# Kernel optimization log

Hardware: AMD Instinct MI355X
Metric: run time of the kernel (lower is better)

## Reference

```python
import jax, jax.numpy as jnp
import numpy as np

N_NODES = 100000


def sage_conv(x, src, dst, Wl, Wr, b):
    # mean-aggregate neighbor (source) features onto destinations
    msg = x[src]                                              # [E, F]
    agg = jax.ops.segment_sum(msg, dst, num_segments=N_NODES)  # [N, F]
    deg = jax.ops.segment_sum(jnp.ones(dst.shape, x.dtype), dst, num_segments=N_NODES)
    agg = agg / jnp.maximum(deg, 1.0)[:, None]
    # PyG SAGEConv: lin_l(aggr) + lin_r(x); bias only on lin_l
    return agg @ Wl.T + x @ Wr.T + b


def setup_inputs() -> dict:
    key = jax.random.key(0)
    ks = jax.random.split(key, 12)
    d, h, c = 128, 128, 6
    s = 1.0 / np.sqrt(d)
    return {
        "x": jax.random.normal(ks[0], (N_NODES, d), jnp.float32),
        "edge_index": jax.random.randint(ks[1], (2, 3200000), 0, N_NODES, jnp.int64),
        "Wl1": jax.random.normal(ks[2], (h, d), jnp.float32) * s,
        "Wr1": jax.random.normal(ks[3], (h, d), jnp.float32) * s,
        "b1": jax.random.normal(ks[4], (h,), jnp.float32) * s,
        "Wl2": jax.random.normal(ks[5], (h, h), jnp.float32) * s,
        "Wr2": jax.random.normal(ks[6], (h, h), jnp.float32) * s,
        "b2": jax.random.normal(ks[7], (h,), jnp.float32) * s,
        "Wl3": jax.random.normal(ks[8], (c, h), jnp.float32) * s,
        "Wr3": jax.random.normal(ks[9], (c, h), jnp.float32) * s,
        "b3": jax.random.normal(ks[10], (c,), jnp.float32) * s,
    }


def reference(x, edge_index, Wl1, Wr1, b1, Wl2, Wr2, b2, Wl3, Wr3, b3):
    src, dst = edge_index[0], edge_index[1]
    h = jax.nn.relu(sage_conv(x, src, dst, Wl1, Wr1, b1))  # dropout = identity (eval)
    h = jax.nn.relu(sage_conv(h, src, dst, Wl2, Wr2, b2))
    return sage_conv(h, src, dst, Wl3, Wr3, b3)  # [N, 6]
```

## Files before the change

### kernel.cpp

```cpp
#include <hip/hip_runtime.h>
#include <hip/hip_bf16.h>

#define N_NODES 100000
#define G_PART 16
#define B_PART 96
#define NPG_PAD 6272
#define A_BLOCKS 1024

__global__ __launch_bounds__(256) void partition_edges(
    const int* __restrict__ src, const int* __restrict__ dst, int E,
    int* __restrict__ bkt, unsigned int* __restrict__ gcur, int cap, int npg) {
    __shared__ int cnt16[G_PART];
    __shared__ unsigned int base16[G_PART];
    __shared__ unsigned int cur16[G_PART];
    int tid = threadIdx.x;
    if (tid < G_PART) cnt16[tid] = 0;
    __syncthreads();
    int per = (E + A_BLOCKS - 1) / A_BLOCKS;
    int beg = blockIdx.x * per;
    int end = min(beg + per, E);
    for (int i = beg + tid; i < end; i += 256) {
        int d = dst[i];
        atomicAdd(&cnt16[d / npg], 1);
    }
    __syncthreads();
    if (tid < G_PART) {
        base16[tid] = atomicAdd(&gcur[tid], (unsigned int)cnt16[tid]);
        cur16[tid] = 0;
    }
    __syncthreads();
    for (int i = beg + tid; i < end; i += 256) {
        int d = dst[i];
        int s = src[i];
        int g = d / npg;
        unsigned int p = base16[g] + atomicAdd(&cur16[g], 1u);
        bkt[(size_t)g * cap + p] = ((d - g * npg) << 17) | s;
    }
}

__global__ __launch_bounds__(256) void count_hist(const int* __restrict__ bkt,
                                                  const unsigned int* __restrict__ gcur,
                                                  int cap, unsigned short* __restrict__ partial,
                                                  int npg, int N) {
    __shared__ int hist[NPG_PAD];
    int g = blockIdx.x & (G_PART - 1);
    int b = blockIdx.x / G_PART;
    int tid = threadIdx.x;
    for (int i = tid; i < npg; i += 256) hist[i] = 0;
    __syncthreads();
    int len = (int)gcur[g];
    int per = (len + B_PART - 1) / B_PART;
    int ibeg = b * per;
    int iend = min(ibeg + per, len);
    const int* bp = bkt + (size_t)g * cap;
    for (int i = ibeg + tid; i < iend; i += 256) {
        int v = __builtin_nontemporal_load(bp + i);
        atomicAdd(&hist[v >> 17], 1);
    }
    __syncthreads();
    size_t base = (size_t)(g * B_PART + b) * npg;
    for (int j = tid; j < npg; j += 256) partial[base + j] = (unsigned short)hist[j];
}

__global__ __launch_bounds__(256) void scan_partials(unsigned short* __restrict__ partial,
                                                     int* __restrict__ cnt,
                                                     int npg, int N) {
    int n = blockIdx.x * 256 + threadIdx.x;
    if (n >= N) return;
    int g = n / npg;
    int i = n - g * npg;
    size_t base = (size_t)g * B_PART * npg + i;
    int run = 0;
#pragma unroll 4
    for (int b = 0; b < B_PART; ++b) {
        size_t idx = base + (size_t)b * npg;
        int t = partial[idx];
        partial[idx] = (unsigned short)run;
        run += t;
    }
    cnt[n] = run;
}

__global__ __launch_bounds__(256) void fill_hist(const int* __restrict__ bkt,
                                                 const unsigned int* __restrict__ gcur,
                                                 int cap,
                                                 const unsigned short* __restrict__ partial,
                                                 const int* __restrict__ row_off,
                                                 int* __restrict__ csr_src,
                                                 int npg, int N) {
    __shared__ int cur[NPG_PAD];
    int g = blockIdx.x & (G_PART - 1);
    int b = blockIdx.x / G_PART;
    int lo = g * npg;
    int tid = threadIdx.x;
    size_t pbase = (size_t)(g * B_PART + b) * npg;
    for (int i = tid; i < npg && lo + i < N; i += 256)
        cur[i] = row_off[lo + i] + (int)partial[pbase + i];
    __syncthreads();
    int len = (int)gcur[g];
    int per = (len + B_PART - 1) / B_PART;
    int ibeg = b * per;
    int iend = min(ibeg + per, len);
    const int* bp = bkt + (size_t)g * cap;
    for (int i = ibeg + tid; i < iend; i += 256) {
        int v = __builtin_nontemporal_load(bp + i);
        int p = atomicAdd(&cur[v >> 17], 1);
        csr_src[p] = v & 0x1FFFF;
    }
}

#define SCHUNK 1024

__global__ __launch_bounds__(256) void scan_blocks(const int* __restrict__ cnt,
                                                   int* __restrict__ row_off,
                                                   int* __restrict__ block_sums, int n) {
    __shared__ int ts[256];
    int tid = threadIdx.x;
    int base = blockIdx.x * SCHUNK + tid * 4;
    int v[4];
    int s = 0;
#pragma unroll
    for (int j = 0; j < 4; ++j) {
        int i = base + j;
        v[j] = (i < n) ? cnt[i] : 0;
        s += v[j];
    }
    ts[tid] = s;
    __syncthreads();
    for (int off = 1; off < 256; off <<= 1) {
        int t = 0;
        if (tid >= off) t = ts[tid - off];
        __syncthreads();
        if (tid >= off) ts[tid] += t;
        __syncthreads();
    }
    int run = (tid > 0) ? ts[tid - 1] : 0;
    if (tid == 255) block_sums[blockIdx.x] = ts[255];
#pragma unroll
    for (int j = 0; j < 4; ++j) {
        int i = base + j;
        if (i < n) row_off[i] = run;
        run += v[j];
    }
}

__global__ __launch_bounds__(256) void scan_sums(int* __restrict__ block_sums, int nb,
                                                 int* __restrict__ row_off, int n) {
    __shared__ int ts[256];
    int tid = threadIdx.x;
    int v = (tid < nb) ? block_sums[tid] : 0;
    ts[tid] = v;
    __syncthreads();
    for (int off = 1; off < 256; off <<= 1) {
        int t = 0;
        if (tid >= off) t = ts[tid - off];
        __syncthreads();
        if (tid >= off) ts[tid] += t;
        __syncthreads();
    }
    if (tid < nb) block_sums[tid] = (tid > 0) ? ts[tid - 1] : 0;
    if (tid == 255) row_off[n] = ts[255];
}

__global__ __launch_bounds__(256) void scan_add(int* __restrict__ row_off,
                                                const int* __restrict__ block_sums, int n) {
    int tid = threadIdx.x;
    int off = block_sums[blockIdx.x];
    int base = blockIdx.x * SCHUNK + tid * 4;
#pragma unroll
    for (int j = 0; j < 4; ++j) {
        int i = base + j;
        if (i < n) row_off[i] += off;
    }
}

__global__ __launch_bounds__(256) void pack_bf16(const float* __restrict__ in,
                                                 uint2* __restrict__ out, int n4) {
    int i = blockIdx.x * 256 + threadIdx.x;
    if (i >= n4) return;
    float4 v = *(const float4*)&in[(size_t)i * 4];
    __hip_bfloat162 p0 = __float22bfloat162_rn(make_float2(v.x, v.y));
    __hip_bfloat162 p1 = __float22bfloat162_rn(make_float2(v.z, v.w));
    uint2 o;
    o.x = *(const uint*)&p0;
    o.y = *(const uint*)&p1;
    out[i] = o;
}

static __device__ inline unsigned short f2bf(float v) {
    __hip_bfloat16 b = __float2bfloat16(v);
    return *(const unsigned short*)&b;
}

__global__ __launch_bounds__(256) void pack_weights(
    const float* __restrict__ Wl1, const float* __restrict__ Wr1,
    const float* __restrict__ Wl2, const float* __restrict__ Wr2,
    const float* __restrict__ Wl3, const float* __restrict__ Wr3,
    unsigned short* __restrict__ Wc1, unsigned short* __restrict__ Wc2,
    unsigned short* __restrict__ W3c) {
    int idx = blockIdx.x * 256 + threadIdx.x;
    if (idx < 32768) {
        int n = idx >> 8, k = idx & 255;
        Wc1[idx] = f2bf((k < 128) ? Wl1[n * 128 + k] : Wr1[n * 128 + (k - 128)]);
    } else if (idx < 65536) {
        int t = idx - 32768;
        int n = t >> 8, k = t & 255;
        Wc2[t] = f2bf((k < 128) ? Wl2[n * 128 + k] : Wr2[n * 128 + (k - 128)]);
    } else if (idx < 65536 + 2048) {
        int t = idx - 65536;
        int n = t >> 7, k = t & 127;
        float v = (n < 6) ? Wl3[n * 128 + k] : ((n < 12) ? Wr3[(n - 6) * 128 + k] : 0.f);
        W3c[t] = f2bf(v);
    }
}

static __device__ inline float2 unpack2(uint v) {
    float2 r;
    r.x = __uint_as_float(v << 16);
    r.y = __uint_as_float(v & 0xffff0000u);
    return r;
}

__global__ __launch_bounds__(256) void agg_bf16(const uint* __restrict__ featb,
                                                const int* __restrict__ row_off,
                                                const int* __restrict__ csr,
                                                uint* __restrict__ outb, int M) {
    int node = blockIdx.x * 4 + (threadIdx.x >> 6);
    if (node >= M) return;
    int lane = threadIdx.x & 63;
    int beg = row_off[node], end = row_off[node + 1];
    float sx = 0.f, sy = 0.f;
    int i = beg;
    for (; i + 4 <= end; i += 4) {
        int s0 = csr[i], s1 = csr[i + 1], s2 = csr[i + 2], s3 = csr[i + 3];
        uint v0 = featb[(size_t)s0 * 64 + lane];
        uint v1 = featb[(size_t)s1 * 64 + lane];
        uint v2 = featb[(size_t)s2 * 64 + lane];
        uint v3 = featb[(size_t)s3 * 64 + lane];
        float2 f0 = unpack2(v0), f1 = unpack2(v1), f2 = unpack2(v2), f3 = unpack2(v3);
        sx += f0.x + f1.x + f2.x + f3.x;
        sy += f0.y + f1.y + f2.y + f3.y;
    }
    for (; i < end; ++i) {
        uint v = featb[(size_t)csr[i] * 64 + lane];
        float2 f = unpack2(v);
        sx += f.x;
        sy += f.y;
    }
    float inv = (end > beg) ? 1.0f / (float)(end - beg) : 0.0f;
    __hip_bfloat162 p = __float22bfloat162_rn(make_float2(sx * inv, sy * inv));
    outb[(size_t)node * 64 + lane] = *(const uint*)&p;
}

typedef __attribute__((ext_vector_type(8))) short bfrag8;
typedef __attribute__((ext_vector_type(4))) float f32x4;

__global__ __launch_bounds__(256) void gemm_mfma(
    const unsigned short* __restrict__ Aagg,
    const unsigned short* __restrict__ Aself,
    const unsigned short* __restrict__ Wc,
    const float* __restrict__ bias,
    unsigned short* __restrict__ outb,
    int M, int relu) {
    int wave = threadIdx.x >> 6;
    int lane = threadIdx.x & 63;
    int m0 = blockIdx.x * 64 + wave * 16;
    int mrow = lane & 15;
    int quad = lane >> 4;
    int row = m0 + mrow;
    int rclamp = (row < M) ? row : 0;

    f32x4 acc[8];
#pragma unroll
    for (int t = 0; t < 8; ++t) acc[t] = (f32x4){0.f, 0.f, 0.f, 0.f};

    const unsigned short* arow0 = Aagg + (size_t)rclamp * 128;
    const unsigned short* arow1 = Aself + (size_t)rclamp * 128;
#pragma unroll
    for (int ks = 0; ks < 8; ++ks) {
        int k0 = ks * 32;
        const unsigned short* ap =
            (k0 < 128) ? (arow0 + k0 + quad * 8) : (arow1 + (k0 - 128) + quad * 8);
        bfrag8 af = *(const bfrag8*)ap;
#pragma unroll
        for (int t = 0; t < 8; ++t) {
            const unsigned short* bp = Wc + (size_t)(t * 16 + mrow) * 256 + k0 + quad * 8;
            bfrag8 bf = *(const bfrag8*)bp;
            acc[t] = __builtin_amdgcn_mfma_f32_16x16x32_bf16(af, bf, acc[t], 0, 0, 0);
        }
    }
#pragma unroll
    for (int t = 0; t < 8; ++t) {
        int col = t * 16 + mrow;
        float bcol = bias[col];
#pragma unroll
        for (int r = 0; r < 4; ++r) {
            int orow = m0 + quad * 4 + r;
            if (orow < M) {
                float v = acc[t][r] + bcol;
                if (relu) v = fmaxf(v, 0.f);
                outb[(size_t)orow * 128 + col] = f2bf(v);
            }
        }
    }
}

__global__ __launch_bounds__(256) void lin3_mfma(
    const unsigned short* __restrict__ h2b,
    const unsigned short* __restrict__ W3c,
    const float* __restrict__ b3,
    unsigned short* __restrict__ zg,
    float* __restrict__ zs,
    int M) {
    int wave = threadIdx.x >> 6;
    int lane = threadIdx.x & 63;
    int m0 = blockIdx.x * 64 + wave * 16;
    int mrow = lane & 15;
    int quad = lane >> 4;
    int row = m0 + mrow;
    int rclamp = (row < M) ? row : 0;
    f32x4 acc = (f32x4){0.f, 0.f, 0.f, 0.f};
    const unsigned short* arow = h2b + (size_t)rclamp * 128;
#pragma unroll
    for (int ks = 0; ks < 4; ++ks) {
        bfrag8 af = *(const bfrag8*)(arow + ks * 32 + quad * 8);
        bfrag8 bf = *(const bfrag8*)(W3c + (size_t)mrow * 128 + ks * 32 + quad * 8);
        acc = __builtin_amdgcn_mfma_f32_16x16x32_bf16(af, bf, acc, 0, 0, 0);
    }
    int col = mrow;
#pragma unroll
    for (int r = 0; r < 4; ++r) {
        int orow = m0 + quad * 4 + r;
        if (orow < M) {
            float v = acc[r];
            if (col < 6) {
                zg[(size_t)orow * 8 + col] = f2bf(v);
            } else if (col < 12) {
                zs[(size_t)orow * 6 + (col - 6)] = v + b3[col - 6];
            }
        }
    }
}

__global__ void out_kernel(const unsigned short* __restrict__ zg,
                           const float* __restrict__ zs,
                           const int* __restrict__ row_off,
                           const int* __restrict__ csr,
                           float* __restrict__ out, int M) {
    int idx = blockIdx.x * blockDim.x + threadIdx.x;
    int node = idx >> 3;
    int j = idx & 7;
    if (node >= M || j >= 6) return;
    int beg = row_off[node], end = row_off[node + 1];
    float acc = 0.f;
    int i = beg;
    for (; i + 4 <= end; i += 4) {
        int s0 = csr[i], s1 = csr[i + 1], s2 = csr[i + 2], s3 = csr[i + 3];
        uint z0 = zg[(size_t)s0 * 8 + j];
        uint z1 = zg[(size_t)s1 * 8 + j];
        uint z2 = zg[(size_t)s2 * 8 + j];
        uint z3 = zg[(size_t)s3 * 8 + j];
        acc += __uint_as_float(z0 << 16) + __uint_as_float(z1 << 16) +
               __uint_as_float(z2 << 16) + __uint_as_float(z3 << 16);
    }
    for (; i < end; ++i) {
        uint z = zg[(size_t)csr[i] * 8 + j];
        acc += __uint_as_float(z << 16);
    }
    float inv = (end > beg) ? 1.0f / (float)(end - beg) : 0.0f;
    out[(size_t)node * 6 + j] = acc * inv + zs[(size_t)node * 6 + j];
}

static inline size_t align_up(size_t x, size_t a) { return (x + a - 1) & ~(a - 1); }

extern "C" void kernel_launch(void* const* d_in, const int* in_sizes, int n_in,
                              void* d_out, int out_size, void* d_ws, size_t ws_size,
                              hipStream_t stream) {
    const float* x = (const float*)d_in[0];
    const int* ei = (const int*)d_in[1];
    const float* Wl1 = (const float*)d_in[2];
    const float* Wr1 = (const float*)d_in[3];
    const float* b1 = (const float*)d_in[4];
    const float* Wl2 = (const float*)d_in[5];
    const float* Wr2 = (const float*)d_in[6];
    const float* b2 = (const float*)d_in[7];
    const float* Wl3 = (const float*)d_in[8];
    const float* Wr3 = (const float*)d_in[9];
    const float* b3 = (const float*)d_in[10];

    const int N = in_sizes[0] / 128;
    const int E = in_sizes[1] / 2;
    const int* src = ei;
    const int* dst = ei + E;

    char* ws = (char*)d_ws;
    size_t off = 0;
    int* cnt = (int*)(ws + off);        off = align_up(off + (size_t)N * 4, 512);
    int* row_off = (int*)(ws + off);    off = align_up(off + (size_t)(N + 1) * 4, 512);
    int* block_sums = (int*)(ws + off); off = align_up(off + 512 * 4, 512);
    unsigned int* gcur = (unsigned int*)(ws + off); off = align_up(off + 64 * 4, 512);
    unsigned short* Wc1 = (unsigned short*)(ws + off); off = align_up(off + 128 * 256 * 2, 512);
    unsigned short* Wc2 = (unsigned short*)(ws + off); off = align_up(off + 128 * 256 * 2, 512);
    unsigned short* W3c = (unsigned short*)(ws + off); off = align_up(off + 16 * 128 * 2, 512);
    int* csr_src = (int*)(ws + off);    off = align_up(off + (size_t)E * 4, 512);
    float* slotA = (float*)(ws + off);  off = align_up(off + (size_t)N * 128 * 4, 512);
    float* slotB = (float*)(ws + off);  off = align_up(off + (size_t)N * 128 * 4, 512);
    float* slotC = (float*)(ws + off);  off = align_up(off + (size_t)N * 128 * 4, 512);
    uint2* h1b = (uint2*)(ws + off);    off = align_up(off + (size_t)N * 128 * 2, 512);
    unsigned short* partial = (unsigned short*)slotA;
    uint* aggb = (uint*)slotA;
    const int cap = 210000;
    int* bkt = (int*)slotB;
    unsigned short* h2b = (unsigned short*)slotB;
    uint2* xb = (uint2*)slotC;
    unsigned short* zg = (unsigned short*)slotC;
    float* zs = (float*)((char*)slotC + align_up((size_t)N * 8 * 2, 512));
    (void)ws_size;

    const int npg = (N + G_PART - 1) / G_PART;
    const int build_grid = G_PART * B_PART;

    hipMemsetAsync(gcur, 0, G_PART * 4, stream);
    partition_edges<<<A_BLOCKS, 256, 0, stream>>>(src, dst, E, bkt, gcur, cap, npg);
    count_hist<<<build_grid, 256, 0, stream>>>(bkt, gcur, cap, partial, npg, N);
    scan_partials<<<(N + 255) / 256, 256, 0, stream>>>(partial, cnt, npg, N);

    const int nscan = (N + SCHUNK - 1) / SCHUNK;
    scan_blocks<<<nscan, 256, 0, stream>>>(cnt, row_off, block_sums, N);
    scan_sums<<<1, 256, 0, stream>>>(block_sums, nscan, row_off, N);
    scan_add<<<nscan, 256, 0, stream>>>(row_off, block_sums, N);

    fill_hist<<<build_grid, 256, 0, stream>>>(bkt, gcur, cap, partial, row_off,
                                              csr_src, npg, N);

    const int n4 = N * 32;
    pack_bf16<<<(n4 + 255) / 256, 256, 0, stream>>>(x, xb, n4);
    pack_weights<<<(65536 + 2048 + 255) / 256, 256, 0, stream>>>(
        Wl1, Wr1, Wl2, Wr2, Wl3, Wr3, Wc1, Wc2, W3c);

    int aggGrid = (N + 3) / 4;
    int gemmGrid = (N + 63) / 64;

    agg_bf16<<<aggGrid, 256, 0, stream>>>((const uint*)xb, row_off, csr_src, aggb, N);
    gemm_mfma<<<gemmGrid, 256, 0, stream>>>((const unsigned short*)aggb,
                                            (const unsigned short*)xb, Wc1, b1,
                                            (unsigned short*)h1b, N, 1);
    agg_bf16<<<aggGrid, 256, 0, stream>>>((const uint*)h1b, row_off, csr_src, aggb, N);
    gemm_mfma<<<gemmGrid, 256, 0, stream>>>((const unsigned short*)aggb,
                                            (const unsigned short*)h1b, Wc2, b2,
                                            h2b, N, 1);
    lin3_mfma<<<gemmGrid, 256, 0, stream>>>(h2b, W3c, b3, zg, zs, N);
    out_kernel<<<(N * 8 + 255) / 256, 256, 0, stream>>>(zg, zs, row_off, csr_src,
                                                        (float*)d_out, N);
}
```

Measured before the change: 615.2 us.

## Fuse neighbor aggregation with layer GEMM and layer-3 projection per tile

Merges the gather-mean aggregation kernel with the following MFMA GEMM, so each 16-node block aggregates into shared memory and immediately multiplies, with no round trip of the aggregated features through global memory. The second layer also computes the layer-3 linear projection in-block and never writes h2 to global memory, which removes two kernel launches and an intermediate buffer. The cost is that every block of 16 nodes reloads the full weight matrix, and each wave now covers only two output tiles instead of all eight. Block occupancy also now depends on the mixed aggregation and GEMM work.

```diff
diff --git a/kernel.cpp b/kernel.cpp
--- a/kernel.cpp
+++ b/kernel.cpp
@@ -214,6 +214,9 @@
     }
 }
 
+typedef __attribute__((ext_vector_type(8))) short bfrag8;
+typedef __attribute__((ext_vector_type(4))) float f32x4;
+
 static __device__ inline float2 unpack2(uint v) {
     float2 r;
     r.x = __uint_as_float(v << 16);
@@ -221,122 +224,114 @@
     return r;
 }
 
-__global__ __launch_bounds__(256) void agg_bf16(const uint* __restrict__ featb,
-                                                const int* __restrict__ row_off,
-                                                const int* __restrict__ csr,
-                                                uint* __restrict__ outb, int M) {
-    int node = blockIdx.x * 4 + (threadIdx.x >> 6);
-    if (node >= M) return;
-    int lane = threadIdx.x & 63;
-    int beg = row_off[node], end = row_off[node + 1];
-    float sx = 0.f, sy = 0.f;
-    int i = beg;
-    for (; i + 4 <= end; i += 4) {
-        int s0 = csr[i], s1 = csr[i + 1], s2 = csr[i + 2], s3 = csr[i + 3];
-        uint v0 = featb[(size_t)s0 * 64 + lane];
-        uint v1 = featb[(size_t)s1 * 64 + lane];
-        uint v2 = featb[(size_t)s2 * 64 + lane];
-        uint v3 = featb[(size_t)s3 * 64 + lane];
-        float2 f0 = unpack2(v0), f1 = unpack2(v1), f2 = unpack2(v2), f3 = unpack2(v3);
-        sx += f0.x + f1.x + f2.x + f3.x;
-        sy += f0.y + f1.y + f2.y + f3.y;
-    }
-    for (; i < end; ++i) {
-        uint v = featb[(size_t)csr[i] * 64 + lane];
-        float2 f = unpack2(v);
-        sx += f.x;
-        sy += f.y;
-    }
-    float inv = (end > beg) ? 1.0f / (float)(end - beg) : 0.0f;
-    __hip_bfloat162 p = __float22bfloat162_rn(make_float2(sx * inv, sy * inv));
-    outb[(size_t)node * 64 + lane] = *(const uint*)&p;
-}
-
-typedef __attribute__((ext_vector_type(8))) short bfrag8;
-typedef __attribute__((ext_vector_type(4))) float f32x4;
-
-__global__ __launch_bounds__(256) void gemm_mfma(
-    const unsigned short* __restrict__ Aagg,
+__global__ __launch_bounds__(256) void agg_gemm(
+    const uint* __restrict__ featb,
     const unsigned short* __restrict__ Aself,
+    const int* __restrict__ row_off,
+    const int* __restrict__ csr,
     const unsigned short* __restrict__ Wc,
     const float* __restrict__ bias,
     unsigned short* __restrict__ outb,
-    int M, int relu) {
-    int wave = threadIdx.x >> 6;
-    int lane = threadIdx.x & 63;
-    int m0 = blockIdx.x * 64 + wave * 16;
-    int mrow = lane & 15;
-    int quad = lane >> 4;
-    int row = m0 + mrow;
-    int rclamp = (row < M) ? row : 0;
-
-    f32x4 acc[8];
-#pragma unroll
-    for (int t = 0; t < 8; ++t) acc[t] = (f32x4){0.f, 0.f, 0.f, 0.f};
-
-    const unsigned short* arow0 = Aagg + (size_t)rclamp * 128;
-    const unsigned short* arow1 = Aself + (size_t)rclamp * 128;
-#pragma unroll
-    for (int ks = 0; ks < 8; ++ks) {
-        int k0 = ks * 32;
-        const unsigned short* ap =
-            (k0 < 128) ? (arow0 + k0 + quad * 8) : (arow1 + (k0 - 128) + quad * 8);
-        bfrag8 af = *(const bfrag8*)ap;
-#pragma unroll
-        for (int t = 0; t < 8; ++t) {
-            const unsigned short* bp = Wc + (size_t)(t * 16 + mrow) * 256 + k0 + quad * 8;
-            bfrag8 bf = *(const bfrag8*)bp;
-            acc[t] = __builtin_amdgcn_mfma_f32_16x16x32_bf16(af, bf, acc[t], 0, 0, 0);
-        }
-    }
-#pragma unroll
-    for (int t = 0; t < 8; ++t) {
-        int col = t * 16 + mrow;
-        float bcol = bias[col];
-#pragma unroll
-        for (int r = 0; r < 4; ++r) {
-            int orow = m0 + quad * 4 + r;
-            if (orow < M) {
-                float v = acc[t][r] + bcol;
-                if (relu) v = fmaxf(v, 0.f);
-                outb[(size_t)orow * 128 + col] = f2bf(v);
-            }
-        }
-    }
-}
-
-__global__ __launch_bounds__(256) void lin3_mfma(
-    const unsigned short* __restrict__ h2b,
+    int do_lin3,
     const unsigned short* __restrict__ W3c,
     const float* __restrict__ b3,
     unsigned short* __restrict__ zg,
     float* __restrict__ zs,
-    int M) {
-    int wave = threadIdx.x >> 6;
-    int lane = threadIdx.x & 63;
-    int m0 = blockIdx.x * 64 + wave * 16;
+    int M, int relu) {
+    __shared__ unsigned short aggT[16][136];
+    __shared__ unsigned short h2T[16][136];
+    int tid = threadIdx.x;
+    int wave = tid >> 6;
+    int lane = tid & 63;
+    int tile = blockIdx.x * 16;
+
+    for (int sub = 0; sub < 4; ++sub) {
+        int node = tile + wave * 4 + sub;
+        float sx = 0.f, sy = 0.f;
+        float inv = 0.f;
+        if (node < M) {
+            int beg = row_off[node], end = row_off[node + 1];
+            int i = beg;
+            for (; i + 4 <= end; i += 4) {
+                int s0 = csr[i], s1 = csr[i + 1], s2 = csr[i + 2], s3 = csr[i + 3];
+                uint v0 = featb[(size_t)s0 * 64 + lane];
+                uint v1 = featb[(size_t)s1 * 64 + lane];
+                uint v2 = featb[(size_t)s2 * 64 + lane];
+                uint v3 = featb[(size_t)s3 * 64 + lane];
+                float2 f0 = unpack2(v0), f1 = unpack2(v1);
+                float2 f2 = unpack2(v2), f3 = unpack2(v3);
+                sx += f0.x + f1.x + f2.x + f3.x;
+                sy += f0.y + f1.y + f2.y + f3.y;
+            }
+            for (; i < end; ++i) {
+                uint v = featb[(size_t)csr[i] * 64 + lane];
+                float2 f = unpack2(v);
+                sx += f.x;
+                sy += f.y;
+            }
+            inv = (end > beg) ? 1.0f / (float)(end - beg) : 0.0f;
+        }
+        __hip_bfloat162 p = __float22bfloat162_rn(make_float2(sx * inv, sy * inv));
+        *(uint*)&aggT[wave * 4 + sub][lane * 2] = *(const uint*)&p;
+    }
+    __syncthreads();
+
     int mrow = lane & 15;
     int quad = lane >> 4;
-    int row = m0 + mrow;
-    int rclamp = (row < M) ? row : 0;
-    f32x4 acc = (f32x4){0.f, 0.f, 0.f, 0.f};
-    const unsigned short* arow = h2b + (size_t)rclamp * 128;
-#pragma unroll
-    for (int ks = 0; ks < 4; ++ks) {
-        bfrag8 af = *(const bfrag8*)(arow + ks * 32 + quad * 8);
-        bfrag8 bf = *(const bfrag8*)(W3c + (size_t)mrow * 128 + ks * 32 + quad * 8);
-        acc = __builtin_amdgcn_mfma_f32_16x16x32_bf16(af, bf, acc, 0, 0, 0);
-    }
-    int col = mrow;
-#pragma unroll
-    for (int r = 0; r < 4; ++r) {
-        int orow = m0 + quad * 4 + r;
-        if (orow < M) {
-            float v = acc[r];
-            if (col < 6) {
-                zg[(size_t)orow * 8 + col] = f2bf(v);
-            } else if (col < 12) {
-                zs[(size_t)orow * 6 + (col - 6)] = v + b3[col - 6];
+    int row = tile + mrow;
+    int rc = (row < M) ? row : 0;
+    f32x4 acc0 = (f32x4){0.f, 0.f, 0.f, 0.f};
+    f32x4 acc1 = (f32x4){0.f, 0.f, 0.f, 0.f};
+    const unsigned short* arow1 = Aself + (size_t)rc * 128;
+    int t0 = wave * 2, t1 = wave * 2 + 1;
+#pragma unroll
+    for (int ks = 0; ks < 8; ++ks) {
+        bfrag8 af;
+        if (ks < 4) af = *(const bfrag8*)&aggT[mrow][ks * 32 + quad * 8];
+        else af = *(const bfrag8*)(arow1 + (ks - 4) * 32 + quad * 8);
+        bfrag8 bf0 = *(const bfrag8*)(Wc + (size_t)(t0 * 16 + mrow) * 256 + ks * 32 + quad * 8);
+        bfrag8 bf1 = *(const bfrag8*)(Wc + (size_t)(t1 * 16 + mrow) * 256 + ks * 32 + quad * 8);
+        acc0 = __builtin_amdgcn_mfma_f32_16x16x32_bf16(af, bf0, acc0, 0, 0, 0);
+        acc1 = __builtin_amdgcn_mfma_f32_16x16x32_bf16(af, bf1, acc1, 0, 0, 0);
+    }
+#pragma unroll
+    for (int tt = 0; tt < 2; ++tt) {
+        f32x4 a = tt ? acc1 : acc0;
+        int t = wave * 2 + tt;
+        int col = t * 16 + mrow;
+        float bc = bias[col];
+#pragma unroll
+        for (int r = 0; r < 4; ++r) {
+            int orow = tile + quad * 4 + r;
+            float v = a[r] + bc;
+            if (relu) v = fmaxf(v, 0.f);
+            unsigned short hv = f2bf(v);
+            if (outb && orow < M) outb[(size_t)orow * 128 + col] = hv;
+            if (do_lin3) h2T[quad * 4 + r][col] = hv;
+        }
+    }
+    if (do_lin3) {
+        __syncthreads();
+        if (wave == 0) {
+            f32x4 acc = (f32x4){0.f, 0.f, 0.f, 0.f};
+#pragma unroll
+            for (int ks = 0; ks < 4; ++ks) {
+                bfrag8 af = *(const bfrag8*)&h2T[mrow][ks * 32 + quad * 8];
+                bfrag8 bf = *(const bfrag8*)(W3c + (size_t)mrow * 128 + ks * 32 + quad * 8);
+                acc = __builtin_amdgcn_mfma_f32_16x16x32_bf16(af, bf, acc, 0, 0, 0);
+            }
+            int col = mrow;
+#pragma unroll
+            for (int r = 0; r < 4; ++r) {
+                int orow = tile + quad * 4 + r;
+                if (orow < M) {
+                    float v = acc[r];
+                    if (col < 6) {
+                        zg[(size_t)orow * 8 + col] = f2bf(v);
+                    } else if (col < 12) {
+                        zs[(size_t)orow * 6 + (col - 6)] = v + b3[col - 6];
+                    }
+                }
             }
         }
     }
@@ -405,16 +400,13 @@
     int* csr_src = (int*)(ws + off);    off = align_up(off + (size_t)E * 4, 512);
     float* slotA = (float*)(ws + off);  off = align_up(off + (size_t)N * 128 * 4, 512);
     float* slotB = (float*)(ws + off);  off = align_up(off + (size_t)N * 128 * 4, 512);
-    float* slotC = (float*)(ws + off);  off = align_up(off + (size_t)N * 128 * 4, 512);
     uint2* h1b = (uint2*)(ws + off);    off = align_up(off + (size_t)N * 128 * 2, 512);
     unsigned short* partial = (unsigned short*)slotA;
-    uint* aggb = (uint*)slotA;
     const int cap = 210000;
     int* bkt = (int*)slotB;
-    unsigned short* h2b = (unsigned short*)slotB;
-    uint2* xb = (uint2*)slotC;
-    unsigned short* zg = (unsigned short*)slotC;
-    float* zs = (float*)((char*)slotC + align_up((size_t)N * 8 * 2, 512));
+    uint2* xb = (uint2*)slotA;
+    unsigned short* zg = (unsigned short*)slotB;
+    float* zs = (float*)((char*)slotB + align_up((size_t)N * 8 * 2, 512));
     (void)ws_size;
 
     const int npg = (N + G_PART - 1) / G_PART;
@@ -438,18 +430,14 @@
     pack_weights<<<(65536 + 2048 + 255) / 256, 256, 0, stream>>>(
         Wl1, Wr1, Wl2, Wr2, Wl3, Wr3, Wc1, Wc2, W3c);
 
-    int aggGrid = (N + 3) / 4;
-    int gemmGrid = (N + 63) / 64;
-
-    agg_bf16<<<aggGrid, 256, 0, stream>>>((const uint*)xb, row_off, csr_src, aggb, N);
-    gemm_mfma<<<gemmGrid, 256, 0, stream>>>((const unsigned short*)aggb,
-                                            (const unsigned short*)xb, Wc1, b1,
-                                            (unsigned short*)h1b, N, 1);
-    agg_bf16<<<aggGrid, 256, 0, stream>>>((const uint*)h1b, row_off, csr_src, aggb, N);
-    gemm_mfma<<<gemmGrid, 256, 0, stream>>>((const unsigned short*)aggb,
-                                            (const unsigned short*)h1b, Wc2, b2,
-                                            h2b, N, 1);
-    lin3_mfma<<<gemmGrid, 256, 0, stream>>>(h2b, W3c, b3, zg, zs, N);
+    int fusedGrid = (N + 15) / 16;
+
+    agg_gemm<<<fusedGrid, 256, 0, stream>>>(
+        (const uint*)xb, (const unsigned short*)xb, row_off, csr_src, Wc1, b1,
+        (unsigned short*)h1b, 0, nullptr, nullptr, nullptr, nullptr, N, 1);
+    agg_gemm<<<fusedGrid, 256, 0, stream>>>(
+        (const uint*)h1b, (const unsigned short*)h1b, row_off, csr_src, Wc2, b2,
+        nullptr, 1, W3c, b3, zg, zs, N, 1);
     out_kernel<<<(N * 8 + 255) / 256, 256, 0, stream>>>(zg, zs, row_off, csr_src,
                                                         (float*)d_out, N);
 }
```

After: 588.8 us. 4.3% less time.
